# Kernel optimization log

Measured on AMD Instinct MI355X. Metric: run time of the kernel, lower is better.

Reference implementation:

```python
import jax, jax.numpy as jnp
import numpy as np
from jax import lax

EPS = 1e-5

def _conv(x, w, pad):
    # x: NCHW, w: OIHW, stride 1
    return lax.conv_general_dilated(x, w, (1, 1), [(pad, pad), (pad, pad)],
                                    dimension_numbers=('NCHW', 'OIHW', 'NCHW'))

def _binconv(x, w):
    # IR-Net/ReActNet HardBinaryConv: sign-binarized weights scaled by per-filter
    # mean |w| (alpha), sign-binarized activations; clip-based STE for backward.
    alpha = jnp.mean(jnp.abs(w), axis=(1, 2, 3), keepdims=True)  # [O,1,1,1]
    wc = jnp.clip(w, -1.0, 1.0)
    bw = lax.stop_gradient(alpha * jnp.sign(w) - wc) + wc
    xc = jnp.clip(x, -1.0, 1.0)
    ba = lax.stop_gradient(jnp.sign(x) - xc) + xc
    return _conv(ba, bw, 1)

def _bn(x, g, b, m, v):
    # inference-mode BatchNorm2d with running stats
    inv = g / jnp.sqrt(v + EPS)
    return x * inv[None, :, None, None] + (b - m * inv)[None, :, None, None]

def _pool(x):
    return lax.reduce_window(x, -jnp.inf, lax.max, (1, 1, 2, 2), (1, 1, 2, 2), 'VALID')

def _htanh(x):
    return jnp.clip(x, -1.0, 1.0)

def setup_inputs() -> dict:
    key = jax.random.key(0)
    ks = jax.random.split(key, 40)
    B = 256
    d = {'x': jax.random.normal(ks[0], (B, 3, 32, 32), jnp.float32)}
    shapes = [(128, 3, 3, 3), (128, 128, 3, 3), (256, 128, 3, 3),
              (256, 256, 3, 3), (512, 256, 3, 3), (512, 512, 3, 3)]
    chans = [128, 128, 256, 256, 512, 512]
    ki = 1
    for i, (ws, c) in enumerate(zip(shapes, chans)):
        fan_in = ws[1] * 9
        d[f'w{i}'] = jax.random.normal(ks[ki], ws, jnp.float32) / np.sqrt(fan_in); ki += 1
        d[f'g{i}'] = jnp.ones((c,), jnp.float32)
        d[f'b{i}'] = jnp.zeros((c,), jnp.float32)
        d[f'm{i}'] = jax.random.normal(ks[ki], (c,), jnp.float32) * 0.1; ki += 1
        d[f'v{i}'] = jax.random.uniform(ks[ki], (c,), jnp.float32, 0.5, 1.5); ki += 1
    d['fcw'] = jax.random.normal(ks[ki], (10, 512 * 4 * 4), jnp.float32) * 0.01
    d['fcb'] = jnp.zeros((10,), jnp.float32)
    return d

def reference(x, w0, g0, b0, m0, v0, w1, g1, b1, m1, v1, w2, g2, b2, m2, v2,
              w3, g3, b3, m3, v3, w4, g4, b4, m4, v4, w5, g5, b5, m5, v5,
              fcw, fcb):
    h = _bn(_conv(x, w0, 1), g0, b0, m0, v0)            # [B,128,32,32]
    h = _htanh(_bn(_pool(_binconv(h, w1)), g1, b1, m1, v1))   # [B,128,16,16]
    h = _htanh(_bn(_binconv(h, w2), g2, b2, m2, v2))          # [B,256,16,16]
    h = _htanh(_bn(_pool(_binconv(h, w3)), g3, b3, m3, v3))   # [B,256,8,8]
    h = _htanh(_bn(_binconv(h, w4), g4, b4, m4, v4))          # [B,512,8,8]
    h = _htanh(_bn(_pool(_binconv(h, w5)), g5, b5, m5, v5))   # [B,512,4,4]
    h = h.reshape(h.shape[0], -1)                             # [B,8192]
    return h @ fcw.T + fcb                                    # [B,10]
```

## Files before the change

### kernel.cpp

```cpp
#include <hip/hip_runtime.h>
#include <cstdint>

#define EPS 1e-5
typedef unsigned long long u64;
typedef unsigned int u32;
typedef unsigned short u16;
typedef int v4i __attribute__((ext_vector_type(4)));

struct BnArgs { const float *g[6], *b[6], *m[6], *v[6]; };
struct PackArgs { const float* w[5]; u64* wbt[5]; };

__global__ void bn_prep_all(BnArgs p, double* __restrict__ scale_all,
                            double* __restrict__ shift_all) {
    int i = blockIdx.x * 256 + threadIdx.x;
    if (i >= 1792) return;
    int l, base;
    if (i < 128)       { l = 0; base = 0; }
    else if (i < 256)  { l = 1; base = 128; }
    else if (i < 512)  { l = 2; base = 256; }
    else if (i < 768)  { l = 3; base = 512; }
    else if (i < 1280) { l = 4; base = 768; }
    else               { l = 5; base = 1280; }
    const int c = i - base;
    double inv = (double)p.g[l][c] / sqrt((double)p.v[l][c] + EPS);
    scale_all[i] = inv;
    shift_all[i] = (double)p.b[l][c] - (double)p.m[l][c] * inv;
}

__global__ void zero_out(float* __restrict__ out, int n) {
    int i = blockIdx.x * blockDim.x + threadIdx.x;
    if (i < n) out[i] = 0.f;
}

__global__ void zero_u64(u64* __restrict__ p, size_t n) {
    size_t i = (size_t)blockIdx.x * 256 + threadIdx.x;
    const size_t step = (size_t)gridDim.x * 256;
    for (; i < n; i += step) p[i] = 0ull;
}

__global__ void pack_all(PackArgs pk, const double* __restrict__ scale_all,
                         const double* __restrict__ shift_all,
                         double* __restrict__ A_all,
                         int* __restrict__ tlt_all, int* __restrict__ tgt_all,
                         u32* __restrict__ ct_all, signed char* __restrict__ wi8) {
    const int ob = blockIdx.x;
    const int t = threadIdx.x;
    int l, base, Cin, bnoff, OTOT, ctoff;
    if (ob < 128)       { l = 0; base = 0;    Cin = 128; bnoff = 128;  OTOT = 128; ctoff = 0; }
    else if (ob < 384)  { l = 1; base = 128;  Cin = 128; bnoff = 256;  OTOT = 256; ctoff = 2048; }
    else if (ob < 640)  { l = 2; base = 384;  Cin = 256; bnoff = 512;  OTOT = 256; ctoff = 6144; }
    else if (ob < 1152) { l = 3; base = 640;  Cin = 256; bnoff = 768;  OTOT = 512; ctoff = 10240; }
    else                { l = 4; base = 1152; Cin = 512; bnoff = 1280; OTOT = 512; ctoff = 18432; }
    const int o = ob - base;
    const float* wo = pk.w[l] + (size_t)o * Cin * 9;

    double s = 0.0;
    for (int k = t; k < Cin * 9; k += 256) s += fabs((double)wo[k]);
    __shared__ double red[256];
    __shared__ u32 stp[9];
    red[t] = s;
    if (t < 9) stp[t] = 0;
    __syncthreads();
    for (int r = 128; r > 0; r >>= 1) {
        if (t < r) red[t] += red[t + r];
        __syncthreads();
    }
    if (t == 0) {
        double alpha = red[0] / (double)(Cin * 9);
        const double dA = alpha * scale_all[bnoff + o];
        const double dB = shift_all[bnoff + o];
        A_all[ob] = dA;
        const int INF = 1 << 30;
        int Tlt, Tgt = INF;
        if (dA > 0.0) {
            const double tt = -dB / dA;
            if (!(fabs(tt) < 6000.0)) {
                Tlt = (dB < 0.0) ? INF : -INF;
            } else {
                int v0 = (int)floor(tt) - 4;
                int c = INF;
                for (int v = v0; v < v0 + 9; ++v)
                    if (fma(dA, (double)v, dB) >= 0.0) { c = v; break; }
                Tlt = c;
            }
        } else if (dA < 0.0) {
            const double tt = -dB / dA;
            if (!(fabs(tt) < 6000.0)) {
                Tlt = (dB < 0.0) ? INF : -INF;
            } else {
                int v0 = (int)floor(tt) - 4;
                int c = INF;
                for (int v = v0; v < v0 + 9; ++v)
                    if (fma(dA, (double)v, dB) < 0.0) { c = v; break; }
                Tlt = -INF;
                Tgt = (c == INF) ? INF : (c - 1);
            }
        } else {
            Tlt = (dB < 0.0) ? INF : -INF;
        }
        tlt_all[ob] = Tlt;
        tgt_all[ob] = Tgt;
    }

    const int W64 = Cin / 64;
    u64* wbt = pk.wbt[l];
    for (int e = t; e < 9 * W64; e += 256) {
        int tap = e / W64, word = e % W64;
        u64 bits = 0;
        for (int j = 0; j < 64; ++j) {
            int c = word * 64 + j;
            if (wo[c * 9 + tap] < 0.f) bits |= (1ull << j);
        }
        wbt[((size_t)tap * OTOT + o) * W64 + word] = bits;
        atomicAdd(&stp[tap], (u32)__popcll(bits));
    }
    if (l == 4) {
        for (int e = t; e < 9 * 512; e += 256) {
            const int tap = e / 512, c = e % 512;
            wi8[((size_t)tap * 512 + o) * 512 + c] =
                (wo[c * 9 + tap] < 0.f) ? (signed char)-1 : (signed char)1;
        }
    }
    __syncthreads();

    if (t < 16) {
        const int pat = t;
        int nv = 0;
        u32 cor = 0;
#pragma unroll
        for (int tap = 0; tap < 9; ++tap) {
            const int dy = tap / 3, dx = tap % 3;
            const bool inv = ((pat & 1) && dy == 0) || ((pat & 2) && dy == 2) ||
                             ((pat & 4) && dx == 0) || ((pat & 8) && dx == 2);
            if (inv) cor += stp[tap]; else nv++;
        }
        ct_all[ctoff + pat * OTOT + o] = (u32)(nv * 64 * W64) + 2u * cor;
    }
}

__global__ __launch_bounds__(256) void conv0_pack(
        const float* __restrict__ x, const float* __restrict__ w0,
        const double* __restrict__ scale, const double* __restrict__ shift,
        u64* __restrict__ bits0) {
    __shared__ double wlds[128 * 27];
    __shared__ double sc[128], sh[128];
    const int tid = threadIdx.x;
    for (int e = tid; e < 128 * 27; e += 256) wlds[e] = (double)w0[e];
    for (int e = tid; e < 128; e += 256) { sc[e] = scale[e]; sh[e] = shift[e]; }
    __syncthreads();

    const int n = blockIdx.y;
    const int p = blockIdx.x * 256 + tid;
    const int y = p >> 5, xx = p & 31;
    const float* xn = x + (size_t)n * 3 * 32 * 32;

    double win[27];
#pragma unroll
    for (int c = 0; c < 3; ++c)
#pragma unroll
        for (int dy = 0; dy < 3; ++dy)
#pragma unroll
            for (int dx = 0; dx < 3; ++dx) {
                const int yy = y + dy - 1, xs = xx + dx - 1;
                const bool ok = (yy >= 0 && yy < 32 && xs >= 0 && xs < 32);
                win[(c * 3 + dy) * 3 + dx] = ok ? (double)xn[(c * 32 + yy) * 32 + xs] : 0.0;
            }

    u64* op = bits0 + (((size_t)n * 34 + (y + 1)) * 34 + (xx + 1)) * 2;
#pragma unroll
    for (int og = 0; og < 2; ++og) {
        u64 word = 0;
#pragma unroll 2
        for (int j = 0; j < 64; ++j) {
            const int o = og * 64 + j;
            const double* wo = &wlds[o * 27];
            double acc = 0.0;
#pragma unroll
            for (int k = 0; k < 27; ++k) acc = fma(wo[k], win[k], acc);
            const double val = acc * sc[o] + sh[o];
            word |= (u64)(val < 0.0) << j;
        }
        op[og] = word;
    }
}

template<int H, int W, int W64, int OTOT, int OPW, bool POOL, bool LAST, int MINW>
__global__ __launch_bounds__(256, MINW) void bconv7(
        const u64* __restrict__ in_bits, const u64* __restrict__ wbt,
        const double* __restrict__ A, const double* __restrict__ B,
        const int* __restrict__ tlt, const int* __restrict__ tgt,
        const u32* __restrict__ ct_all, int ctoff,
        u32* __restrict__ out_bits, float* __restrict__ h5) {
    const int tid = threadIdx.x;
    const int wave = tid >> 6, lane = tid & 63;
    constexpr int WPI = (H * W) / 64;
    const int img = (WPI >= 4) ? blockIdx.z : (blockIdx.z * 4 + wave);
    const int wii = (WPI >= 4) ? (blockIdx.y * 4 + wave) : 0;
    const int y = wii * (64 / W) + lane / W;
    const int x = lane % W;
    const int obase = blockIdx.x * OPW;

    __shared__ u32 ctl[16 * (OPW + 1)];
    for (int e = tid; e < 16 * OPW; e += 256) {
        const int pat = e / OPW, oc = e % OPW;
        ctl[pat * (OPW + 1) + oc] = ct_all[ctoff + pat * OTOT + obase + oc];
    }
    __syncthreads();

    constexpr int RC = W + 2;
    const u64* ib = in_bits + (size_t)img * (H + 2) * RC * W64;

    int acc[OPW];
#pragma unroll
    for (int oc = 0; oc < OPW; ++oc) acc[oc] = 0;

#pragma unroll 1
    for (int dy = 0; dy < 3; ++dy) {
#pragma unroll 1
        for (int dx = 0; dx < 3; ++dx) {
            const u64* q = ib + ((size_t)(y + dy) * RC + (x + dx)) * W64;
            u64 wn[W64];
#pragma unroll
            for (int k = 0; k < W64; ++k) wn[k] = q[k];
            const u64* wt = wbt + (size_t)((dy * 3 + dx) * OTOT + obase) * W64;
#pragma unroll
            for (int oc = 0; oc < OPW; ++oc) {
#pragma unroll
                for (int k = 0; k < W64; ++k)
                    acc[oc] += (int)__popcll(wn[k] ^ wt[oc * W64 + k]);
            }
        }
    }

    const int pat = (y == 0 ? 1 : 0) | (y == H - 1 ? 2 : 0) |
                    (x == 0 ? 4 : 0) | (x == W - 1 ? 8 : 0);
    const int ctbase = pat * (OPW + 1);
    constexpr int Hp = POOL ? H / 2 : H, Wp = POOL ? W / 2 : W;
    const bool writer = (!POOL) || (((lane & 1) == 0) && ((lane & W) == 0));
    const int py = POOL ? (y >> 1) : y, px = POOL ? (x >> 1) : x;

    u32 cur = 0;
#pragma unroll
    for (int oc = 0; oc < OPW; ++oc) {
        int v = (int)ctl[ctbase + oc] - 2 * acc[oc];
        if (POOL) {
            int v2 = max(v, __shfl_xor(v, 1, 64));
            v = max(v2, __shfl_xor(v2, W, 64));
        }
        if (LAST) {
            const double t = fma(A[obase + oc], (double)v, B[obase + oc]);
            const double hcl = fmin(1.0, fmax(-1.0, t));
            if (writer)
                h5[(((size_t)img * OTOT + obase + oc) * Hp + py) * Wp + px] = (float)hcl;
        } else {
            const bool bit = (v < tlt[obase + oc]) | (v > tgt[obase + oc]);
            cur |= (u32)bit << oc;
        }
    }
    if (!LAST && writer) {
        const size_t wordIdx =
            (((size_t)img * (Hp + 2) + (py + 1)) * (Wp + 2) + (px + 1)) * (OTOT / 32)
            + (obase >> 5);
        if (OPW == 32) {
            out_bits[wordIdx] = cur;
        } else {
            u16* o16 = (u16*)out_bits;
            o16[wordIdx * 2 + ((obase >> 4) & 1)] = (u16)cur;
        }
    }
}

__global__ __launch_bounds__(256, 2) void bconv5_mfma(
        const u64* __restrict__ bits4, const signed char* __restrict__ wi8,
        const double* __restrict__ A, const double* __restrict__ B,
        float* __restrict__ h5) {
    const int tid = threadIdx.x;
    const int wave = tid >> 6, lane = tid & 63;
    const int img = blockIdx.y;
    const int nhalf = blockIdx.x;

    __shared__ __align__(16) signed char act[100 * 528];
    {
        u32* a32 = (u32*)act;
        for (int e = tid; e < 100 * 132; e += 256) a32[e] = 0;
        __syncthreads();
        for (int e = tid; e < 64 * 128; e += 256) {
            const int px = e >> 7, wi = e & 127;
            const int cell = (px >> 3) * 10 + (px & 7) + 11;
            const u64 bb = bits4[((size_t)img * 100 + cell) * 8 + (wi >> 4)];
            const u32 nib = (u32)(bb >> ((wi & 15) * 4)) & 0xF;
            const u32 spread = (nib & 1) | ((nib & 2) << 7) |
                               ((nib & 4) << 14) | ((nib & 8) << 21);
            a32[cell * 132 + wi] = 0x01010101u + 254u * spread;
        }
    }
    __syncthreads();

    const int r16 = lane & 15, kg4 = lane >> 4;
    const int ntb = nhalf * 16 + wave * 4;

    v4i acc[4][4];
#pragma unroll
    for (int m = 0; m < 4; ++m)
#pragma unroll
        for (int q = 0; q < 4; ++q) acc[m][q] = (v4i){0, 0, 0, 0};

    int acell[4];
#pragma unroll
    for (int m = 0; m < 4; ++m) {
        const int px = m * 16 + r16;
        acell[m] = ((px >> 3) + (m * 2 - (px >> 3) ? 0 : 0)) * 10 + (px & 7);
        acell[m] = (m * 2 + (r16 >> 3)) * 10 + (r16 & 7);
    }

#pragma unroll 1
    for (int tap = 0; tap < 9; ++tap) {
        const int coff = (tap / 3) * 10 + (tap % 3);
        const signed char* wb = wi8 + (size_t)tap * 512 * 512;
#pragma unroll 1
        for (int kg = 0; kg < 8; ++kg) {
            const int kofs = kg * 64 + kg4 * 16;
            v4i af[4];
#pragma unroll
            for (int m = 0; m < 4; ++m)
                af[m] = *(const v4i*)&act[(acell[m] + coff) * 528 + kofs];
#pragma unroll
            for (int q = 0; q < 4; ++q) {
                const int oc = (ntb + q) * 16 + r16;
                const v4i bf = *(const v4i*)&wb[(size_t)oc * 512 + kofs];
#pragma unroll
                for (int m = 0; m < 4; ++m)
                    acc[m][q] = __builtin_amdgcn_mfma_i32_16x16x64_i8(
                        af[m], bf, acc[m][q], 0, 0, 0);
            }
        }
    }

#pragma unroll
    for (int m = 0; m < 4; ++m) {
#pragma unroll
        for (int q = 0; q < 4; ++q) {
            const int v01 = max(acc[m][q][0], acc[m][q][1]);
            const int v23 = max(acc[m][q][2], acc[m][q][3]);
            const int p0 = max(v01, __shfl_xor(v01, 32, 64));
            const int p1 = max(v23, __shfl_xor(v23, 32, 64));
            if (kg4 < 2) {
                const int oc = (ntb + q) * 16 + r16;
                const int py = m;
                const int px0 = kg4 * 2;
                const double Av = A[oc], Bv = B[oc];
                const double t0 = fma(Av, (double)p0, Bv);
                const double t1 = fma(Av, (double)p1, Bv);
                float* hp = &h5[(((size_t)img * 512 + oc) * 4 + py) * 4 + px0];
                hp[0] = (float)fmin(1.0, fmax(-1.0, t0));
                hp[1] = (float)fmin(1.0, fmax(-1.0, t1));
            }
        }
    }
}

__global__ void fc_kernel(const float* __restrict__ h, const float* __restrict__ fcw,
                          const float* __restrict__ fcb, float* __restrict__ out) {
    const int n = blockIdx.x, t = threadIdx.x;
    double acc[10];
#pragma unroll
    for (int j = 0; j < 10; ++j) acc[j] = 0.0;
    const float* hn = h + (size_t)n * 8192;
    for (int k = t; k < 8192; k += 256) {
        double xv = (double)hn[k];
#pragma unroll
        for (int j = 0; j < 10; ++j) acc[j] += xv * (double)fcw[j * 8192 + k];
    }
    __shared__ double red[10][256];
#pragma unroll
    for (int j = 0; j < 10; ++j) red[j][t] = acc[j];
    __syncthreads();
    for (int r = 128; r > 0; r >>= 1) {
        if (t < r) {
#pragma unroll
            for (int j = 0; j < 10; ++j) red[j][t] += red[j][t + r];
        }
        __syncthreads();
    }
    if (t < 10) out[n * 10 + t] = (float)(red[t][0] + (double)fcb[t]);
}

extern "C" void kernel_launch(void* const* d_in, const int* in_sizes, int n_in,
                              void* d_out, int out_size, void* d_ws, size_t ws_size,
                              hipStream_t stream) {
    const float* X = (const float*)d_in[0];
    BnArgs bn;
    PackArgs pk;
    const float* Wt0 = (const float*)d_in[1];
    for (int i = 0; i < 6; ++i) {
        bn.g[i] = (const float*)d_in[2 + 5 * i];
        bn.b[i] = (const float*)d_in[3 + 5 * i];
        bn.m[i] = (const float*)d_in[4 + 5 * i];
        bn.v[i] = (const float*)d_in[5 + 5 * i];
    }
    for (int i = 0; i < 5; ++i) pk.w[i] = (const float*)d_in[1 + 5 * (i + 1)];
    const float* fcw = (const float*)d_in[31];
    const float* fcb = (const float*)d_in[32];
    float* out = (float*)d_out;

    char* ws = (char*)d_ws;
    size_t off = 0;
    auto alloc = [&](size_t bytes) -> void* {
        void* p = ws + off;
        off = (off + bytes + 255) & ~(size_t)255;
        return p;
    };

    double* scale_all = (double*)alloc(1792 * sizeof(double));
    double* shift_all = (double*)alloc(1792 * sizeof(double));
    double* A_all     = (double*)alloc(1664 * sizeof(double));
    int* tlt_all      = (int*)alloc(1664 * sizeof(int));
    int* tgt_all      = (int*)alloc(1664 * sizeof(int));
    u32* ct_all       = (u32*)alloc(26624 * sizeof(u32));
    signed char* wi8  = (signed char*)alloc(9ull * 512 * 512);
    const size_t WBN[5] = {128ull * 9 * 2, 256ull * 9 * 2, 256ull * 9 * 4,
                           512ull * 9 * 4, 512ull * 9 * 8};
    for (int i = 0; i < 5; ++i) pk.wbt[i] = (u64*)alloc(WBN[i] * sizeof(u64));
    u64* bits4 = (u64*)alloc(256ull * 10 * 10 * 8 * sizeof(u64));
    u64* bits0 = (u64*)alloc(256ull * 34 * 34 * 2 * sizeof(u64));
    u64* bits1 = (u64*)alloc(256ull * 18 * 18 * 2 * sizeof(u64));
    u64* bits2 = (u64*)alloc(256ull * 18 * 18 * 4 * sizeof(u64));
    u64* bits3 = (u64*)alloc(256ull * 10 * 10 * 4 * sizeof(u64));
    const size_t bits_u64 =
        256ull * (10 * 10 * 8 + 34 * 34 * 2 + 18 * 18 * 2 + 18 * 18 * 4 + 10 * 10 * 4);
    float* h5 = (float*)bits0;
    {
        const size_t h5_bytes = 256ull * 8192 * sizeof(float);
        const size_t have = (size_t)((char*)(bits3 + 256ull * 10 * 10 * 4) - (char*)bits0);
        if (h5_bytes > have) alloc(h5_bytes - have);
    }

    if (off > ws_size) {
        zero_out<<<dim3((out_size + 255) / 256), dim3(256), 0, stream>>>(out, out_size);
        return;
    }

    const int BOF[6] = {0, 128, 256, 512, 768, 1280};
    const int AOF[5] = {0, 128, 384, 640, 1152};
    const int CTO[5] = {0, 2048, 6144, 10240, 18432};

    bn_prep_all<<<dim3(7), dim3(256), 0, stream>>>(bn, scale_all, shift_all);
    pack_all<<<dim3(1664), dim3(256), 0, stream>>>(pk, scale_all, shift_all,
                                                   A_all, tlt_all, tgt_all, ct_all, wi8);
    zero_u64<<<dim3(2048), dim3(256), 0, stream>>>(bits4, bits_u64);

    conv0_pack<<<dim3(4, 256), dim3(256), 0, stream>>>(
        X, Wt0, scale_all + BOF[0], shift_all + BOF[0], bits0);

    bconv7<32, 32, 2, 128, 32, true, false, 4><<<dim3(4, 4, 256), dim3(256), 0, stream>>>(
        bits0, pk.wbt[0], nullptr, nullptr, tlt_all + AOF[0], tgt_all + AOF[0],
        ct_all, CTO[0], (u32*)bits1, nullptr);
    bconv7<16, 16, 2, 256, 32, false, false, 4><<<dim3(8, 1, 256), dim3(256), 0, stream>>>(
        bits1, pk.wbt[1], nullptr, nullptr, tlt_all + AOF[1], tgt_all + AOF[1],
        ct_all, CTO[1], (u32*)bits2, nullptr);
    bconv7<16, 16, 4, 256, 32, true, false, 4><<<dim3(8, 1, 256), dim3(256), 0, stream>>>(
        bits2, pk.wbt[2], nullptr, nullptr, tlt_all + AOF[2], tgt_all + AOF[2],
        ct_all, CTO[2], (u32*)bits3, nullptr);
    bconv7<8, 8, 4, 512, 16, false, false, 8><<<dim3(32, 1, 64), dim3(256), 0, stream>>>(
        bits3, pk.wbt[3], nullptr, nullptr, tlt_all + AOF[3], tgt_all + AOF[3],
        ct_all, CTO[3], (u32*)bits4, nullptr);

    bconv5_mfma<<<dim3(2, 256), dim3(256), 0, stream>>>(
        bits4, wi8, A_all + AOF[4], shift_all + BOF[5], h5);

    fc_kernel<<<dim3(256), dim3(256), 0, stream>>>(h5, fcw, fcb, out);
}
```

Measured before the change: 574.1 us.

## Software-pipeline bconv5 MFMA loop and split output channels over more blocks

The final binary conv kernel now double-buffers its LDS activation fragments and global weight fragments across a flattened 72-step tap/k loop, so the loads for the next step are issued while the current MFMAs run. Each wave handles 2 output tiles instead of 4, the grid doubles to 4 blocks per image, and launch bounds rise to 3 blocks per CU for higher occupancy and less latency exposure. The cost is that every block repeats the LDS activation unpack, and activation fragments are reused across fewer output tiles.

```diff
diff --git a/kernel.cpp b/kernel.cpp
--- a/kernel.cpp
+++ b/kernel.cpp
@@ -270,14 +270,14 @@
     }
 }
 
-__global__ __launch_bounds__(256, 2) void bconv5_mfma(
+__global__ __launch_bounds__(256, 3) void bconv5_mfma(
         const u64* __restrict__ bits4, const signed char* __restrict__ wi8,
         const double* __restrict__ A, const double* __restrict__ B,
         float* __restrict__ h5) {
     const int tid = threadIdx.x;
     const int wave = tid >> 6, lane = tid & 63;
     const int img = blockIdx.y;
-    const int nhalf = blockIdx.x;
+    const int ntb = blockIdx.x * 8 + wave * 2;
 
     __shared__ __align__(16) signed char act[100 * 528];
     {
@@ -297,49 +297,63 @@
     __syncthreads();
 
     const int r16 = lane & 15, kg4 = lane >> 4;
-    const int ntb = nhalf * 16 + wave * 4;
-
-    v4i acc[4][4];
+    const int klane = kg4 * 16;
+
+    int acell[4];
 #pragma unroll
     for (int m = 0; m < 4; ++m)
-#pragma unroll
-        for (int q = 0; q < 4; ++q) acc[m][q] = (v4i){0, 0, 0, 0};
-
-    int acell[4];
+        acell[m] = (m * 2 + (r16 >> 3)) * 10 + (r16 & 7);
+
+    const signed char* wbL = wi8 + (size_t)ntb * 8192 + (size_t)r16 * 512;
+
+    v4i acc[4][2];
+#pragma unroll
+    for (int m = 0; m < 4; ++m)
+#pragma unroll
+        for (int q = 0; q < 2; ++q) acc[m][q] = (v4i){0, 0, 0, 0};
+
+    auto loadA = [&](int it, v4i* af) {
+        const int tap = it >> 3, kg = it & 7;
+        const int t3 = (tap * 11) >> 5;
+        const int coff = t3 * 10 + (tap - t3 * 3);
+        const int kofs = kg * 64 + klane;
+#pragma unroll
+        for (int m = 0; m < 4; ++m)
+            af[m] = *(const v4i*)&act[(acell[m] + coff) * 528 + kofs];
+    };
+    auto loadB = [&](int it, v4i* bf) {
+        const int tap = it >> 3, kg = it & 7;
+        const size_t base = (size_t)tap * 262144 + (size_t)(kg * 64 + klane);
+#pragma unroll
+        for (int q = 0; q < 2; ++q)
+            bf[q] = *(const v4i*)&wbL[base + (size_t)q * 8192];
+    };
+
+    v4i afA[4], bfA[2], afB[4], bfB[2];
+    loadA(0, afA); loadB(0, bfA);
+
+#pragma unroll 1
+    for (int it = 0; it < 72; it += 2) {
+        loadA(it + 1, afB); loadB(it + 1, bfB);
+#pragma unroll
+        for (int q = 0; q < 2; ++q)
+#pragma unroll
+            for (int m = 0; m < 4; ++m)
+                acc[m][q] = __builtin_amdgcn_mfma_i32_16x16x64_i8(
+                    afA[m], bfA[q], acc[m][q], 0, 0, 0);
+        if (it + 2 < 72) { loadA(it + 2, afA); loadB(it + 2, bfA); }
+#pragma unroll
+        for (int q = 0; q < 2; ++q)
+#pragma unroll
+            for (int m = 0; m < 4; ++m)
+                acc[m][q] = __builtin_amdgcn_mfma_i32_16x16x64_i8(
+                    afB[m], bfB[q], acc[m][q], 0, 0, 0);
+    }
+
 #pragma unroll
     for (int m = 0; m < 4; ++m) {
-        const int px = m * 16 + r16;
-        acell[m] = ((px >> 3) + (m * 2 - (px >> 3) ? 0 : 0)) * 10 + (px & 7);
-        acell[m] = (m * 2 + (r16 >> 3)) * 10 + (r16 & 7);
-    }
-
-#pragma unroll 1
-    for (int tap = 0; tap < 9; ++tap) {
-        const int coff = (tap / 3) * 10 + (tap % 3);
-        const signed char* wb = wi8 + (size_t)tap * 512 * 512;
-#pragma unroll 1
-        for (int kg = 0; kg < 8; ++kg) {
-            const int kofs = kg * 64 + kg4 * 16;
-            v4i af[4];
-#pragma unroll
-            for (int m = 0; m < 4; ++m)
-                af[m] = *(const v4i*)&act[(acell[m] + coff) * 528 + kofs];
-#pragma unroll
-            for (int q = 0; q < 4; ++q) {
-                const int oc = (ntb + q) * 16 + r16;
-                const v4i bf = *(const v4i*)&wb[(size_t)oc * 512 + kofs];
-#pragma unroll
-                for (int m = 0; m < 4; ++m)
-                    acc[m][q] = __builtin_amdgcn_mfma_i32_16x16x64_i8(
-                        af[m], bf, acc[m][q], 0, 0, 0);
-            }
-        }
-    }
-
-#pragma unroll
-    for (int m = 0; m < 4; ++m) {
-#pragma unroll
-        for (int q = 0; q < 4; ++q) {
+#pragma unroll
+        for (int q = 0; q < 2; ++q) {
             const int v01 = max(acc[m][q][0], acc[m][q][1]);
             const int v23 = max(acc[m][q][2], acc[m][q][3]);
             const int p0 = max(v01, __shfl_xor(v01, 32, 64));
@@ -465,7 +479,7 @@
         bits3, pk.wbt[3], nullptr, nullptr, tlt_all + AOF[3], tgt_all + AOF[3],
         ct_all, CTO[3], (u32*)bits4, nullptr);
 
-    bconv5_mfma<<<dim3(2, 256), dim3(256), 0, stream>>>(
+    bconv5_mfma<<<dim3(4, 256), dim3(256), 0, stream>>>(
         bits4, wi8, A_all + AOF[4], shift_all + BOF[5], h5);
 
     fc_kernel<<<dim3(256), dim3(256), 0, stream>>>(h5, fcw, fcb, out);
```

Measured after the change: 603.0 us. +5.0%, slower.
